# Kernel tuning notes

Hardware: AMD Instinct MI355X
Metric: run time of the kernel (lower is better)

The kernel has to match this reference:

```python
import jax, jax.numpy as jnp
import numpy as np
import math

B, L, H, V, NH, HD, FF, NL = 4096, 64, 64, 21, 4, 16, 128, 2


def _ln(x, g, b, eps=1e-6):
    mu = jnp.mean(x, axis=-1, keepdims=True)
    var = jnp.mean(jnp.square(x - mu), axis=-1, keepdims=True)
    return g * (x - mu) * jax.lax.rsqrt(var + eps) + b


def _pe():
    # standard sinusoidal positional encoding (L, H)
    pos = np.arange(L, dtype=np.float32)[:, None]
    div = np.exp(np.arange(0, H, 2, dtype=np.float32) * (-math.log(10000.0) / H))
    pe = np.zeros((L, H), dtype=np.float32)
    pe[:, 0::2] = np.sin(pos * div)
    pe[:, 1::2] = np.cos(pos * div)
    return jnp.asarray(pe)


def _soft_assemble(soft_mask, digit_values):
    # differentiable base-10 assembly: weight digit i by 10^(#digits to its right)
    cum = jnp.cumsum(soft_mask, axis=1)
    tot = jnp.sum(soft_mask, axis=1, keepdims=True)
    w = jnp.power(10.0, (tot - cum) * soft_mask) * soft_mask
    return jnp.sum(digit_values * w, axis=1, keepdims=True)  # (B,1)


def _fixed_ops(l, r):
    add = l + r
    sub = l - r
    mul = l * r
    bad = jnp.abs(r) < 1e-6
    div = jnp.where(bad, 0.0, l / jnp.where(bad, 1.0, r))
    ones = jnp.ones_like(l)
    dvalid = (~bad).astype(l.dtype)
    results = jnp.stack([add, sub, mul, div], axis=1)   # (B,4,1)
    valids = jnp.stack([ones, ones, ones, dvalid], axis=1)
    return results, valids


def _forward(token_ids, emb, np_w, np_b, grp_wq, grp_bq, grp_wk, grp_bk, grp_ln_g, grp_ln_b,
             attn_w, attn_b, ln1_g, ln1_b, ln2_g, ln2_b, ffn_w1, ffn_b1, ffn_w2, ffn_b2,
             enc_g, enc_b, red_w, red_b, opc_w, opc_b, res_w, res_b, soft_op):
    mask = (token_ids != 0).astype(jnp.float32)                     # (B,L)
    idsf = token_ids.astype(jnp.float32)
    is_digit = ((token_ids >= 4) & (token_ids <= 13)).astype(jnp.float32)
    digit_values = (idsf - 4.0) * is_digit
    is_op = (token_ids >= 14) & (token_ids <= 17)
    op_type = jnp.where(is_op, idsf - 13.0, 0.0)                    # 14->1 .. 17->4
    is_operator = is_op.astype(jnp.float32)
    num_feat = jnp.stack([digit_values, is_digit, op_type, is_operator], axis=-1)  # (B,L,4)

    x = emb[token_ids] * math.sqrt(H) + num_feat @ np_w + np_b      # (B,L,H)
    x = x + _pe()

    eye = jnp.eye(L, dtype=jnp.float32)
    adj = jnp.eye(L, k=1, dtype=jnp.float32) + jnp.eye(L, k=-1, dtype=jnp.float32)
    tri = jnp.triu(jnp.ones((L, L), jnp.float32))
    a_up = jnp.eye(L, k=1, dtype=jnp.float32)
    pairmask = mask[:, :, None] * mask[:, None, :]

    prior = jnp.float32(0.0)
    for i in range(NL):
        # --- Tree-Transformer group (constituent) attention ---
        c = _ln(x, grp_ln_g[i], grp_ln_b[i])
        q = c @ grp_wq[i] + grp_bq[i]
        k = c @ grp_wk[i] + grp_bk[i]
        s = jnp.einsum('bid,bjd->bij', q, k) / math.sqrt(H)
        gm = adj[None] * pairmask
        s = jnp.where(gm > 0, s, -1e9)
        nb = jax.nn.softmax(s, axis=-1)
        nb = jnp.sqrt(nb * jnp.swapaxes(nb, -1, -2) + 1e-9)
        nb = prior + (1.0 - prior) * nb
        t = (jnp.log(nb + 1e-9) * a_up[None]) @ tri
        g = jnp.exp(tri @ t) * (tri - eye)[None]
        g = g + jnp.swapaxes(g, -1, -2) + jnp.where(eye[None] > 0, nb, 1e-9)  # (B,L,L)
        # --- multi-head attention weighted by group prob (pre-norm residual) ---
        h = _ln(x, ln1_g[i], ln1_b[i])
        def proj(w, b):
            return (h @ w + b).reshape(B, L, NH, HD).transpose(0, 2, 1, 3)
        qh, kh, vh = proj(attn_w[i, 0], attn_b[i, 0]), proj(attn_w[i, 1], attn_b[i, 1]), proj(attn_w[i, 2], attn_b[i, 2])
        sc = jnp.einsum('bhid,bhjd->bhij', qh, kh) / math.sqrt(HD)
        sc = jnp.where(mask[:, None, None, :] > 0, sc, -1e9)
        p = jax.nn.softmax(sc, axis=-1) * g[:, None]
        o = jnp.einsum('bhij,bhjd->bhid', p, vh).transpose(0, 2, 1, 3).reshape(B, L, H)
        x = x + (o @ attn_w[i, 3] + attn_b[i, 3])
        # --- FFN ---
        h2 = _ln(x, ln2_g[i], ln2_b[i])
        x = x + (jax.nn.relu(h2 @ ffn_w1[i] + ffn_b1[i]) @ ffn_w2[i] + ffn_b2[i])
        prior = g

    x = _ln(x, enc_g, enc_b)
    scores = jnp.squeeze(x @ red_w + red_b, -1) + (1.0 - mask) * -1e9
    rw = jax.nn.softmax(scores, axis=-1)                            # reduction weights (B,L)
    cum = jnp.cumsum(rw, axis=1)
    left_mask = (1.0 - cum) * is_digit
    right_mask = (cum - rw) * is_digit
    left_val = _soft_assemble(left_mask, digit_values)
    right_val = _soft_assemble(right_mask, digit_values)
    pooled = jnp.sum(x * rw[..., None], axis=1)                     # (B,H)
    op_logits = pooled @ opc_w + opc_b
    op_probs = jax.nn.softmax(op_logits, axis=-1)
    all_res, all_val = _fixed_ops(left_val, right_val)
    if soft_op:
        w = op_probs[..., None]
    else:
        w = jax.nn.one_hot(jnp.argmax(op_probs, axis=-1), 4)[..., None]
    result = jnp.sum(all_res * w, axis=1)                           # (B,1)
    valid = jnp.sum(all_val * w, axis=1)
    rc = jnp.sign(result) * jnp.log1p(jnp.abs(result))
    result_embedding = jnp.concatenate([rc, valid], axis=-1) @ res_w + res_b  # (B,H)
    return result, result_embedding, valid, left_val, right_val, op_logits, rw


def setup_inputs() -> dict:
    key = jax.random.key(0)
    ks = jax.random.split(key, 16)
    s = 0.05
    rn = lambda k, shape: jax.random.normal(k, shape, dtype=jnp.float32) * s
    z = lambda shape: jnp.zeros(shape, jnp.float32)
    o = lambda shape: jnp.ones(shape, jnp.float32)
    return {
        'token_ids': jax.random.randint(ks[0], (B, L), 0, V, dtype=jnp.int32),
        'emb': rn(ks[1], (V, H)),
        'np_w': rn(ks[2], (4, H)), 'np_b': z((H,)),
        'grp_wq': rn(ks[3], (NL, H, H)), 'grp_bq': z((NL, H)),
        'grp_wk': rn(ks[4], (NL, H, H)), 'grp_bk': z((NL, H)),
        'grp_ln_g': o((NL, H)), 'grp_ln_b': z((NL, H)),
        'attn_w': rn(ks[5], (NL, 4, H, H)), 'attn_b': z((NL, 4, H)),
        'ln1_g': o((NL, H)), 'ln1_b': z((NL, H)),
        'ln2_g': o((NL, H)), 'ln2_b': z((NL, H)),
        'ffn_w1': rn(ks[6], (NL, H, FF)), 'ffn_b1': z((NL, FF)),
        'ffn_w2': rn(ks[7], (NL, FF, H)), 'ffn_b2': z((NL, H)),
        'enc_g': o((H,)), 'enc_b': z((H,)),
        'red_w': rn(ks[8], (H, 1)), 'red_b': z((1,)),
        'opc_w': rn(ks[9], (H, 4)), 'opc_b': z((4,)),
        'res_w': rn(ks[10], (2, H)), 'res_b': z((H,)),
    }


def reference(token_ids, emb, np_w, np_b, grp_wq, grp_bq, grp_wk, grp_bk, grp_ln_g, grp_ln_b,
              attn_w, attn_b, ln1_g, ln1_b, ln2_g, ln2_b, ffn_w1, ffn_b1, ffn_w2, ffn_b2,
              enc_g, enc_b, red_w, red_b, opc_w, opc_b, res_w, res_b):
    # inference path (training=None): hard argmax op select
    return _forward(token_ids, emb, np_w, np_b, grp_wq, grp_bq, grp_wk, grp_bk, grp_ln_g, grp_ln_b,
                    attn_w, attn_b, ln1_g, ln1_b, ln2_g, ln2_b, ffn_w1, ffn_b1, ffn_w2, ffn_b2,
                    enc_g, enc_b, red_w, red_b, opc_w, opc_b, res_w, res_b, soft_op=False)
```

## Files before the change

### kernel.cpp

```cpp
#include <hip/hip_runtime.h>
#include <math.h>

constexpr int BATCH = 4096;

constexpr int A    = 0;
constexpr int B0   = 4352;
constexpr int PS   = B0;
constexpr int PSQ  = B0 + 256;
constexpr int BH   = B0 + 512;
constexpr int MB   = 9024;
constexpr int M_MASK = MB + 0;
constexpr int M_DVAL = MB + 64;
constexpr int M_ISD  = MB + 128;
constexpr int M_SD   = MB + 192;
constexpr int M_NBU  = MB + 256;
constexpr int M_DG   = MB + 320;
constexpr int M_DVEC = MB + 384;
constexpr int M_S    = MB + 448;
constexpr int M_PRU  = MB + 512;
constexpr int M_PRD  = MB + 576;
constexpr int M_SU   = MB + 640;
constexpr int M_SDN  = MB + 704;
constexpr int LDSN   = MB + 768;

constexpr int O_RES   = 0;
constexpr int O_REMB  = 4096;
constexpr int O_VALID = 266240;
constexpr int O_LEFT  = 270336;
constexpr int O_RIGHT = 274432;
constexpr int O_OPL   = 278528;
constexpr int O_RW    = 294912;

#define LN_STORE(GPTR, BPTR, STORE) do {                                  \
    float s_ = 0.f, q_ = 0.f;                                             \
    _Pragma("unroll") for (int j = 0; j < 16; ++j) {                      \
        s_ += xr[j]; q_ = fmaf(xr[j], xr[j], q_); }                       \
    lds[PS  + (wv << 6) + lane] = s_;                                     \
    lds[PSQ + (wv << 6) + lane] = q_;                                     \
    __syncthreads();                                                      \
    float fs_ = lds[PS + lane] + lds[PS + 64 + lane]                      \
              + lds[PS + 128 + lane] + lds[PS + 192 + lane];              \
    float fq_ = lds[PSQ + lane] + lds[PSQ + 64 + lane]                    \
              + lds[PSQ + 128 + lane] + lds[PSQ + 192 + lane];            \
    float mu_ = fs_ * 0.015625f;                                          \
    float inv_ = rsqrtf(fq_ * 0.015625f - mu_ * mu_ + 1e-6f);             \
    _Pragma("unroll") for (int j = 0; j < 16; ++j) {                      \
        int c_ = c0 + j;                                                  \
        float hv_ = (xr[j] - mu_) * inv_ * (GPTR)[c_] + (BPTR)[c_];       \
        STORE;                                                            \
    }                                                                     \
    __syncthreads();                                                      \
} while (0)

__global__ void __launch_bounds__(256, 4) fsa_kernel(
    const int* __restrict__ tok,
    const float* __restrict__ emb, const float* __restrict__ np_w, const float* __restrict__ np_b,
    const float* __restrict__ grp_wq, const float* __restrict__ grp_bq,
    const float* __restrict__ grp_wk, const float* __restrict__ grp_bk,
    const float* __restrict__ grp_ln_g, const float* __restrict__ grp_ln_b,
    const float* __restrict__ attn_w, const float* __restrict__ attn_b,
    const float* __restrict__ ln1_g, const float* __restrict__ ln1_b,
    const float* __restrict__ ln2_g, const float* __restrict__ ln2_b,
    const float* __restrict__ ffn_w1, const float* __restrict__ ffn_b1,
    const float* __restrict__ ffn_w2, const float* __restrict__ ffn_b2,
    const float* __restrict__ enc_g, const float* __restrict__ enc_b,
    const float* __restrict__ red_w, const float* __restrict__ red_b,
    const float* __restrict__ opc_w, const float* __restrict__ opc_b,
    const float* __restrict__ res_w, const float* __restrict__ res_b,
    float* __restrict__ out)
{
    __shared__ __align__(16) float lds[LDSN];
    const int b = blockIdx.x;
    const int tid = threadIdx.x;
    const int lane = tid & 63;
    const int wv = __builtin_amdgcn_readfirstlane(tid >> 6);
    const int c0 = wv << 4;
    float xr[16];

    {
        int t = tok[(b << 6) + lane];
        float mk  = (t != 0) ? 1.f : 0.f;
        float isd = (t >= 4 && t <= 13) ? 1.f : 0.f;
        float dvv = ((float)t - 4.f) * isd;
        float iso = (t >= 14 && t <= 17) ? 1.f : 0.f;
        float opt = iso * ((float)t - 13.f);
        if (wv == 0) {
            lds[M_MASK + lane] = mk;  lds[M_DVAL + lane] = dvv; lds[M_ISD + lane] = isd;
            lds[M_PRU + lane] = 0.f;  lds[M_PRD + lane] = 0.f;
        }
        const float lg = -0.143911568f;
        #pragma unroll
        for (int j = 0; j < 16; ++j) {
            int c = c0 + j;
            float freq = expf((float)(c & ~1) * lg);
            float ang = (float)lane * freq;
            float pe = (c & 1) ? cosf(ang) : sinf(ang);
            xr[j] = emb[t * 64 + c] * 8.f
                  + dvv * np_w[c] + isd * np_w[64 + c]
                  + opt * np_w[128 + c] + iso * np_w[192 + c]
                  + np_b[c] + pe;
        }
    }
    __syncthreads();
    const unsigned long long mall = __ballot(lds[M_MASK + lane] > 0.f);

    for (int il = 0; il < 2; ++il) {
        const float* gwq = grp_wq + il * 4096; const float* gbq = grp_bq + (il << 6);
        const float* gwk = grp_wk + il * 4096; const float* gbk = grp_bk + (il << 6);
        const float* glg = grp_ln_g + (il << 6); const float* glb = grp_ln_b + (il << 6);
        const float* aw  = attn_w + il * 16384;  const float* ab  = attn_b + (il << 8);
        const float* l1g = ln1_g + (il << 6);    const float* l1b = ln1_b + (il << 6);
        const float* l2g = ln2_g + (il << 6);    const float* l2b = ln2_b + (il << 6);
        const float* fw1 = ffn_w1 + il * 8192;   const float* fb1 = ffn_b1 + (il << 7);
        const float* fw2 = ffn_w2 + il * 8192;   const float* fb2 = ffn_b2 + (il << 6);

        LN_STORE(glg, glb, lds[A + c_ * 64 + lane] = hv_);
        {
            float qa[16], ka[16];
            #pragma unroll
            for (int j = 0; j < 16; ++j) { qa[j] = gbq[c0 + j]; ka[j] = gbk[c0 + j]; }
            #pragma unroll 8
            for (int kk = 0; kk < 64; ++kk) {
                float a = lds[A + kk * 64 + lane];
                const float* wq = gwq + kk * 64 + c0;
                const float* wk = gwk + kk * 64 + c0;
                #pragma unroll
                for (int j = 0; j < 16; ++j) {
                    qa[j] = fmaf(a, wq[j], qa[j]);
                    ka[j] = fmaf(a, wk[j], ka[j]);
                }
            }
            #pragma unroll
            for (int j = 0; j < 16; ++j) lds[B0 + (c0 + j) * 64 + lane] = qa[j];
            __syncthreads();
            #pragma unroll
            for (int j = 0; j < 16; ++j) lds[A + (c0 + j) * 64 + lane] = ka[j];
            __syncthreads();
        }

        if (tid < 126) {
            int i = tid >> 1, w = tid & 1;
            int ra = w ? i + 1 : i, rb = w ? i : i + 1;
            float s = 0.f;
            #pragma unroll 8
            for (int c2 = 0; c2 < 64; ++c2)
                s = fmaf(lds[B0 + c2 * 64 + ra], lds[A + c2 * 64 + rb], s);
            lds[(w ? M_SDN : M_SU) + i] = s * 0.125f;
        }
        __syncthreads();

        if (wv == 0) {
            const int i = lane;
            float mi  = lds[M_MASK + i];
            float mup = (i < 63) ? lds[M_MASK + i + 1] : 0.f;
            float mdn = (i > 0)  ? lds[M_MASK + i - 1] : 0.f;
            float eu = (mi > 0.f && mup > 0.f) ? lds[M_SU + i] : -1e9f;
            float ed = (i > 0 && mi > 0.f && mdn > 0.f) ? lds[M_SDN + i - 1] : -1e9f;
            float m = fmaxf(eu, ed);
            float nu, nd, ng;
            if (m <= -1e9f) { nu = 0.015625f; nd = 0.015625f; ng = 0.015625f; }
            else {
                float zu = __expf(eu - m), zd = __expf(ed - m);
                float iz = 1.f / (zu + zd);
                nu = zu * iz; nd = zd * iz; ng = 0.f;
            }
            float nd1 = __shfl_down(nd, 1);
            float pd = lds[M_PRD + i];
            float dsym = sqrtf(ng * ng + 1e-9f);
            float d2 = pd + (1.f - pd) * dsym;
            lds[M_DVEC + i] = d2; lds[M_PRD + i] = d2;
            float la = 0.f;
            if (i < 63) {
                float pu = lds[M_PRU + i];
                float as_ = sqrtf(nu * nd1 + 1e-9f);
                float a2 = pu + (1.f - pu) * as_;
                la = logf(a2 + 1e-9f);
                lds[M_PRU + i] = __expf(la) + 1e-9f;
            }
            float x = __shfl_up(la, 1);
            if (i == 0) x = 0.f;
            #pragma unroll
            for (int off = 1; off < 64; off <<= 1) {
                float t2 = __shfl_up(x, off);
                if (i >= off) x += t2;
            }
            lds[M_S + i] = x;
        }
        __syncthreads();

        LN_STORE(l1g, l1b, lds[A + c_ * 64 + lane] = hv_);
        {
            const int hb = wv << 4;
            const int TB = B0 + wv * 640;
            const int jl = lane & 15, cq = lane >> 4;
            float qa[16];
            #pragma unroll
            for (int j = 0; j < 16; ++j) qa[j] = ab[hb + j];
            #pragma unroll 8
            for (int kk = 0; kk < 64; ++kk) {
                float a = lds[A + kk * 64 + lane];
                const float* wq = aw + kk * 64 + hb;
                #pragma unroll
                for (int j = 0; j < 16; ++j) qa[j] = fmaf(a, wq[j], qa[j]);
            }
            float o[16];
            #pragma unroll
            for (int c = 0; c < 16; ++c) o[c] = 0.f;
            float mrun = -1e30f, z = 0.f;
            for (int jt = 0; jt < 4; ++jt) {
                {
                    float kacc[4], vacc[4];
                    #pragma unroll
                    for (int j = 0; j < 4; ++j) {
                        kacc[j] = ab[64 + hb + (cq << 2) + j];
                        vacc[j] = ab[128 + hb + (cq << 2) + j];
                    }
                    const int row = (jt << 4) + jl;
                    #pragma unroll 8
                    for (int kk = 0; kk < 64; ++kk) {
                        float a = lds[A + kk * 64 + row];
                        const float* wk  = aw + 4096 + kk * 64 + hb + (cq << 2);
                        const float* wvp = aw + 8192 + kk * 64 + hb + (cq << 2);
                        #pragma unroll
                        for (int j = 0; j < 4; ++j) {
                            kacc[j] = fmaf(a, wk[j], kacc[j]);
                            vacc[j] = fmaf(a, wvp[j], vacc[j]);
                        }
                    }
                    *reinterpret_cast<float4*>(&lds[TB + jl * 20 + (cq << 2)]) =
                        make_float4(kacc[0], kacc[1], kacc[2], kacc[3]);
                    *reinterpret_cast<float4*>(&lds[TB + 320 + jl * 20 + (cq << 2)]) =
                        make_float4(vacc[0], vacc[1], vacc[2], vacc[3]);
                    asm volatile("s_waitcnt lgkmcnt(0)" ::: "memory");
                }
                #pragma unroll
                for (int half = 0; half < 2; ++half) {
                    float sc[8]; float tm = -1e30f;
                    #pragma unroll
                    for (int jj = 0; jj < 8; ++jj) {
                        const int jloc = (half << 3) + jj;
                        const int j = (jt << 4) + jloc;
                        float s = 0.f;
                        #pragma unroll
                        for (int c4 = 0; c4 < 4; ++c4) {
                            const float4 kv = *reinterpret_cast<const float4*>(
                                &lds[TB + jloc * 20 + (c4 << 2)]);
                            s = fmaf(qa[(c4<<2)+0], kv.x, s); s = fmaf(qa[(c4<<2)+1], kv.y, s);
                            s = fmaf(qa[(c4<<2)+2], kv.z, s); s = fmaf(qa[(c4<<2)+3], kv.w, s);
                        }
                        s = ((mall >> j) & 1ull) ? s * 0.25f : -1e9f;
                        sc[jj] = s; tm = fmaxf(tm, s);
                    }
                    float mn = fmaxf(mrun, tm);
                    float rs = __expf(mrun - mn);
                    z *= rs;
                    #pragma unroll
                    for (int c = 0; c < 16; ++c) o[c] *= rs;
                    mrun = mn;
                    float Sr  = lds[M_S + lane];
                    float dvr = lds[M_DVEC + lane];
                    #pragma unroll
                    for (int jj = 0; jj < 8; ++jj) {
                        const int jloc = (half << 3) + jj;
                        const int j = (jt << 4) + jloc;
                        float e = __expf(sc[jj] - mn);
                        z += e;
                        float Sj = lds[M_S + j];
                        float g = (j == lane) ? dvr
                                  : (__expf((j > lane) ? (Sj - Sr) : (Sr - Sj)) + 1e-9f);
                        float w = e * g;
                        #pragma unroll
                        for (int c4 = 0; c4 < 4; ++c4) {
                            const float4 vv = *reinterpret_cast<const float4*>(
                                &lds[TB + 320 + jloc * 20 + (c4 << 2)]);
                            o[(c4<<2)+0] = fmaf(w, vv.x, o[(c4<<2)+0]);
                            o[(c4<<2)+1] = fmaf(w, vv.y, o[(c4<<2)+1]);
                            o[(c4<<2)+2] = fmaf(w, vv.z, o[(c4<<2)+2]);
                            o[(c4<<2)+3] = fmaf(w, vv.w, o[(c4<<2)+3]);
                        }
                    }
                }
            }
            float iz = 1.f / z;
            __syncthreads();
            #pragma unroll
            for (int c = 0; c < 16; ++c) lds[A + lane * 65 + hb + c] = o[c] * iz;
            __syncthreads();
            const float* Wo = aw + 12288; const float* bo = ab + 192;
            float acc[16];
            #pragma unroll
            for (int j = 0; j < 16; ++j) acc[j] = bo[c0 + j];
            #pragma unroll 8
            for (int dd = 0; dd < 64; ++dd) {
                float a = lds[A + lane * 65 + dd];
                const float* wr = Wo + dd * 64 + c0;
                #pragma unroll
                for (int j = 0; j < 16; ++j) acc[j] = fmaf(a, wr[j], acc[j]);
            }
            #pragma unroll
            for (int j = 0; j < 16; ++j) xr[j] += acc[j];
        }
        __syncthreads();

        LN_STORE(l2g, l2b, lds[A + c_ * 64 + lane] = hv_);
        {
            float fa[16];
            #pragma unroll
            for (int j = 0; j < 16; ++j) fa[j] = fb1[c0 + j];
            #pragma unroll 8
            for (int kk = 0; kk < 64; ++kk) {
                float a = lds[A + kk * 64 + lane];
                const float* wr = fw1 + kk * 128 + c0;
                #pragma unroll
                for (int j = 0; j < 16; ++j) fa[j] = fmaf(a, wr[j], fa[j]);
            }
            #pragma unroll
            for (int j = 0; j < 16; ++j) lds[B0 + (c0 + j) * 64 + lane] = fmaxf(fa[j], 0.f);
        }
        __syncthreads();
        {
            float acc[16];
            #pragma unroll
            for (int j = 0; j < 16; ++j) acc[j] = fb2[c0 + j];
            #pragma unroll 8
            for (int kk = 0; kk < 64; ++kk) {
                float a = lds[B0 + kk * 64 + lane];
                const float* wr = fw2 + kk * 64 + c0;
                #pragma unroll
                for (int j = 0; j < 16; ++j) acc[j] = fmaf(a, wr[j], acc[j]);
            }
            #pragma unroll
            for (int j = 0; j < 16; ++j) xr[j] += acc[j];
        }
        __syncthreads();
        {
            float fa[16];
            #pragma unroll
            for (int j = 0; j < 16; ++j) fa[j] = fb1[64 + c0 + j];
            #pragma unroll 8
            for (int kk = 0; kk < 64; ++kk) {
                float a = lds[A + kk * 64 + lane];
                const float* wr = fw1 + kk * 128 + 64 + c0;
                #pragma unroll
                for (int j = 0; j < 16; ++j) fa[j] = fmaf(a, wr[j], fa[j]);
            }
            #pragma unroll
            for (int j = 0; j < 16; ++j) lds[B0 + (c0 + j) * 64 + lane] = fmaxf(fa[j], 0.f);
        }
        __syncthreads();
        {
            float acc[16];
            #pragma unroll
            for (int j = 0; j < 16; ++j) acc[j] = 0.f;
            #pragma unroll 8
            for (int kk = 0; kk < 64; ++kk) {
                float a = lds[B0 + kk * 64 + lane];
                const float* wr = fw2 + (64 + kk) * 64 + c0;
                #pragma unroll
                for (int j = 0; j < 16; ++j) acc[j] = fmaf(a, wr[j], acc[j]);
            }
            #pragma unroll
            for (int j = 0; j < 16; ++j) xr[j] += acc[j];
        }
        __syncthreads();
    }

    LN_STORE(enc_g, enc_b, lds[BH + lane * 65 + c_] = hv_);
    if (tid < 64) {
        float s = 0.f;
        #pragma unroll 8
        for (int c2 = 0; c2 < 64; ++c2)
            s = fmaf(lds[BH + tid * 65 + c2], red_w[c2], s);
        s += red_b[0];
        s += (1.f - lds[M_MASK + tid]) * -1e9f;
        lds[M_SU + tid] = s;
    }
    __syncthreads();

    if (wv == 0) {
        float s = lds[M_SU + lane];
        float m = s;
        #pragma unroll
        for (int off = 1; off < 64; off <<= 1) m = fmaxf(m, __shfl_xor(m, off));
        float ee = expf(s - m);
        float z = ee;
        #pragma unroll
        for (int off = 1; off < 64; off <<= 1) z += __shfl_xor(z, off);
        float rw = ee / z;
        lds[M_SD + lane] = rw;
        float cum = rw;
        #pragma unroll
        for (int off = 1; off < 64; off <<= 1) { float t2 = __shfl_up(cum, off); if (lane >= off) cum += t2; }
        float isd = lds[M_ISD + lane], dvv = lds[M_DVAL + lane];
        float lm = (1.f - cum) * isd;
        float rm = (cum - rw) * isd;
        float cl = lm;
        #pragma unroll
        for (int off = 1; off < 64; off <<= 1) { float t2 = __shfl_up(cl, off); if (lane >= off) cl += t2; }
        float totl = __shfl(cl, 63);
        float wL = powf(10.f, (totl - cl) * lm) * lm;
        float lv = dvv * wL;
        #pragma unroll
        for (int off = 1; off < 64; off <<= 1) lv += __shfl_xor(lv, off);
        float cr = rm;
        #pragma unroll
        for (int off = 1; off < 64; off <<= 1) { float t2 = __shfl_up(cr, off); if (lane >= off) cr += t2; }
        float totr = __shfl(cr, 63);
        float wR = powf(10.f, (totr - cr) * rm) * rm;
        float rv = dvv * wR;
        #pragma unroll
        for (int off = 1; off < 64; off <<= 1) rv += __shfl_xor(rv, off);
        if (lane == 0) { lds[M_DG + 2] = lv; lds[M_DG + 3] = rv; }
    }
    __syncthreads();

    if (tid < 64) {
        float p = 0.f;
        #pragma unroll 8
        for (int r2 = 0; r2 < 64; ++r2)
            p = fmaf(lds[BH + r2 * 65 + tid], lds[M_SD + r2], p);
        lds[M_NBU + tid] = p;
    }
    __syncthreads();
    if (tid < 4) {
        float s = opc_b[tid];
        for (int c2 = 0; c2 < 64; ++c2) s = fmaf(lds[M_NBU + c2], opc_w[(c2 << 2) + tid], s);
        lds[M_DG + 4 + tid] = s;
    }
    __syncthreads();
    if (tid == 0) {
        float l = lds[M_DG + 2], r = lds[M_DG + 3];
        float o0 = lds[M_DG + 4], o1 = lds[M_DG + 5], o2 = lds[M_DG + 6], o3 = lds[M_DG + 7];
        int op = 0; float bm = o0;
        if (o1 > bm) { bm = o1; op = 1; }
        if (o2 > bm) { bm = o2; op = 2; }
        if (o3 > bm) { bm = o3; op = 3; }
        float res, vl = 1.f;
        if (op == 0)      res = l + r;
        else if (op == 1) res = l - r;
        else if (op == 2) res = l * r;
        else { bool bad = fabsf(r) < 1e-6f; res = bad ? 0.f : (l / r); vl = bad ? 0.f : 1.f; }
        float rc = (res > 0.f) ? log1pf(res) : ((res < 0.f) ? -log1pf(-res) : 0.f);
        lds[M_DG + 0] = rc; lds[M_DG + 1] = vl;
        out[O_RES + b]   = res;
        out[O_VALID + b] = vl;
        out[O_LEFT + b]  = l;
        out[O_RIGHT + b] = r;
    }
    __syncthreads();
    if (tid < 64) {
        float rc = lds[M_DG + 0], vl = lds[M_DG + 1];
        out[O_REMB + (b << 6) + tid] = rc * res_w[tid] + vl * res_w[64 + tid] + res_b[tid];
        out[O_RW + (b << 6) + tid] = lds[M_SD + tid];
    }
    if (tid >= 64 && tid < 68) {
        int o = tid - 64;
        out[O_OPL + (b << 2) + o] = lds[M_DG + 4 + o];
    }
}

extern "C" void kernel_launch(void* const* d_in, const int* in_sizes, int n_in,
                              void* d_out, int out_size, void* d_ws, size_t ws_size,
                              hipStream_t stream)
{
    fsa_kernel<<<dim3(BATCH), dim3(256), 0, stream>>>(
        (const int*)d_in[0],
        (const float*)d_in[1],  (const float*)d_in[2],  (const float*)d_in[3],
        (const float*)d_in[4],  (const float*)d_in[5],  (const float*)d_in[6],  (const float*)d_in[7],
        (const float*)d_in[8],  (const float*)d_in[9],  (const float*)d_in[10], (const float*)d_in[11],
        (const float*)d_in[12], (const float*)d_in[13], (const float*)d_in[14], (const float*)d_in[15],
        (const float*)d_in[16], (const float*)d_in[17], (const float*)d_in[18], (const float*)d_in[19],
        (const float*)d_in[20], (const float*)d_in[21], (const float*)d_in[22], (const float*)d_in[23],
        (const float*)d_in[24], (const float*)d_in[25], (const float*)d_in[26], (const float*)d_in[27],
        (float*)d_out);
}
```

Before: 950.4 us.

## Fuse layernorm partial sums into producers, use exp2 softmax, fold op-classifier into readout

Each layernorm's partial-sum pass now runs at the end of the stage that produced x, which removes one block-wide barrier per layernorm. The attention softmax and group-gate exponentials switch to exp2f with the scale folded into a log2e constant. The final pooling and op-classifier matmuls are reassociated: the per-row opc projections are computed together with the reduction scores and then weighted by the readout vector inside a single wave, which removes two barrier-separated serial stages. This adds extra register pressure and relies on the M_S values being stored in log2 units for exp2 to stay equivalent.

```diff
diff --git a/kernel.cpp b/kernel.cpp
--- a/kernel.cpp
+++ b/kernel.cpp
@@ -5,15 +5,14 @@
 
 constexpr int A    = 0;
 constexpr int B0   = 4352;
-constexpr int PS   = B0;
-constexpr int PSQ  = B0 + 256;
-constexpr int BH   = B0 + 512;
+constexpr int PS   = B0 + 4096;
+constexpr int PSQ  = PS + 256;
+constexpr int HOPB = PS;
 constexpr int MB   = 9024;
 constexpr int M_MASK = MB + 0;
 constexpr int M_DVAL = MB + 64;
 constexpr int M_ISD  = MB + 128;
 constexpr int M_SD   = MB + 192;
-constexpr int M_NBU  = MB + 256;
 constexpr int M_DG   = MB + 320;
 constexpr int M_DVEC = MB + 384;
 constexpr int M_S    = MB + 448;
@@ -31,13 +30,15 @@
 constexpr int O_OPL   = 278528;
 constexpr int O_RW    = 294912;
 
-#define LN_STORE(GPTR, BPTR, STORE) do {                                  \
+#define LN_PART() do {                                                    \
     float s_ = 0.f, q_ = 0.f;                                             \
     _Pragma("unroll") for (int j = 0; j < 16; ++j) {                      \
         s_ += xr[j]; q_ = fmaf(xr[j], xr[j], q_); }                       \
     lds[PS  + (wv << 6) + lane] = s_;                                     \
     lds[PSQ + (wv << 6) + lane] = q_;                                     \
-    __syncthreads();                                                      \
+} while (0)
+
+#define LN_APPLY(GPTR, BPTR) do {                                         \
     float fs_ = lds[PS + lane] + lds[PS + 64 + lane]                      \
               + lds[PS + 128 + lane] + lds[PS + 192 + lane];              \
     float fq_ = lds[PSQ + lane] + lds[PSQ + 64 + lane]                    \
@@ -46,10 +47,9 @@
     float inv_ = rsqrtf(fq_ * 0.015625f - mu_ * mu_ + 1e-6f);             \
     _Pragma("unroll") for (int j = 0; j < 16; ++j) {                      \
         int c_ = c0 + j;                                                  \
-        float hv_ = (xr[j] - mu_) * inv_ * (GPTR)[c_] + (BPTR)[c_];       \
-        STORE;                                                            \
+        lds[A + c_ * 64 + lane] =                                         \
+            (xr[j] - mu_) * inv_ * (GPTR)[c_] + (BPTR)[c_];               \
     }                                                                     \
-    __syncthreads();                                                      \
 } while (0)
 
 __global__ void __launch_bounds__(256, 4) fsa_kernel(
@@ -100,6 +100,7 @@
                   + opt * np_w[128 + c] + iso * np_w[192 + c]
                   + np_b[c] + pe;
         }
+        LN_PART();
     }
     __syncthreads();
     const unsigned long long mall = __ballot(lds[M_MASK + lane] > 0.f);
@@ -114,9 +115,11 @@
         const float* fw1 = ffn_w1 + il * 8192;   const float* fb1 = ffn_b1 + (il << 7);
         const float* fw2 = ffn_w2 + il * 8192;   const float* fb2 = ffn_b2 + (il << 6);
 
-        LN_STORE(glg, glb, lds[A + c_ * 64 + lane] = hv_);
-        {
-            float qa[16], ka[16];
+        LN_APPLY(glg, glb);
+        __syncthreads();
+        float ka[16];
+        {
+            float qa[16];
             #pragma unroll
             for (int j = 0; j < 16; ++j) { qa[j] = gbq[c0 + j]; ka[j] = gbk[c0 + j]; }
             #pragma unroll 8
@@ -132,11 +135,11 @@
             }
             #pragma unroll
             for (int j = 0; j < 16; ++j) lds[B0 + (c0 + j) * 64 + lane] = qa[j];
-            __syncthreads();
-            #pragma unroll
-            for (int j = 0; j < 16; ++j) lds[A + (c0 + j) * 64 + lane] = ka[j];
-            __syncthreads();
-        }
+        }
+        __syncthreads();
+        #pragma unroll
+        for (int j = 0; j < 16; ++j) lds[A + (c0 + j) * 64 + lane] = ka[j];
+        __syncthreads();
 
         if (tid < 126) {
             int i = tid >> 1, w = tid & 1;
@@ -149,6 +152,7 @@
         }
         __syncthreads();
 
+        LN_PART();
         if (wv == 0) {
             const int i = lane;
             float mi  = lds[M_MASK + i];
@@ -169,15 +173,15 @@
             float dsym = sqrtf(ng * ng + 1e-9f);
             float d2 = pd + (1.f - pd) * dsym;
             lds[M_DVEC + i] = d2; lds[M_PRD + i] = d2;
-            float la = 0.f;
+            float la2 = 0.f;
             if (i < 63) {
                 float pu = lds[M_PRU + i];
                 float as_ = sqrtf(nu * nd1 + 1e-9f);
                 float a2 = pu + (1.f - pu) * as_;
-                la = logf(a2 + 1e-9f);
-                lds[M_PRU + i] = __expf(la) + 1e-9f;
-            }
-            float x = __shfl_up(la, 1);
+                la2 = __log2f(a2 + 1e-9f);
+                lds[M_PRU + i] = exp2f(la2) + 1e-9f;
+            }
+            float x = __shfl_up(la2, 1);
             if (i == 0) x = 0.f;
             #pragma unroll
             for (int off = 1; off < 64; off <<= 1) {
@@ -188,11 +192,13 @@
         }
         __syncthreads();
 
-        LN_STORE(l1g, l1b, lds[A + c_ * 64 + lane] = hv_);
+        LN_APPLY(l1g, l1b);
+        __syncthreads();
         {
             const int hb = wv << 4;
             const int TB = B0 + wv * 640;
             const int jl = lane & 15, cq = lane >> 4;
+            const float SCL = 0.36067376f;
             float qa[16];
             #pragma unroll
             for (int j = 0; j < 16; ++j) qa[j] = ab[hb + j];
@@ -203,6 +209,8 @@
                 #pragma unroll
                 for (int j = 0; j < 16; ++j) qa[j] = fmaf(a, wq[j], qa[j]);
             }
+            const float Sr2 = lds[M_S + lane];
+            const float dvr = lds[M_DVEC + lane];
             float o[16];
             #pragma unroll
             for (int c = 0; c < 16; ++c) o[c] = 0.f;
@@ -248,26 +256,24 @@
                             s = fmaf(qa[(c4<<2)+0], kv.x, s); s = fmaf(qa[(c4<<2)+1], kv.y, s);
                             s = fmaf(qa[(c4<<2)+2], kv.z, s); s = fmaf(qa[(c4<<2)+3], kv.w, s);
                         }
-                        s = ((mall >> j) & 1ull) ? s * 0.25f : -1e9f;
+                        s = ((mall >> j) & 1ull) ? s * SCL : -1e9f;
                         sc[jj] = s; tm = fmaxf(tm, s);
                     }
                     float mn = fmaxf(mrun, tm);
-                    float rs = __expf(mrun - mn);
+                    float rs = exp2f(mrun - mn);
                     z *= rs;
                     #pragma unroll
                     for (int c = 0; c < 16; ++c) o[c] *= rs;
                     mrun = mn;
-                    float Sr  = lds[M_S + lane];
-                    float dvr = lds[M_DVEC + lane];
                     #pragma unroll
                     for (int jj = 0; jj < 8; ++jj) {
                         const int jloc = (half << 3) + jj;
                         const int j = (jt << 4) + jloc;
-                        float e = __expf(sc[jj] - mn);
+                        float e = exp2f(sc[jj] - mn);
                         z += e;
-                        float Sj = lds[M_S + j];
+                        float Sj2 = lds[M_S + j];
                         float g = (j == lane) ? dvr
-                                  : (__expf((j > lane) ? (Sj - Sr) : (Sr - Sj)) + 1e-9f);
+                                  : (exp2f((j > lane) ? (Sj2 - Sr2) : (Sr2 - Sj2)) + 1e-9f);
                         float w = e * g;
                         #pragma unroll
                         for (int c4 = 0; c4 < 4; ++c4) {
@@ -299,10 +305,12 @@
             }
             #pragma unroll
             for (int j = 0; j < 16; ++j) xr[j] += acc[j];
-        }
-        __syncthreads();
-
-        LN_STORE(l2g, l2b, lds[A + c_ * 64 + lane] = hv_);
+            LN_PART();
+        }
+        __syncthreads();
+
+        LN_APPLY(l2g, l2b);
+        __syncthreads();
         {
             float fa[16];
             #pragma unroll
@@ -361,19 +369,28 @@
             }
             #pragma unroll
             for (int j = 0; j < 16; ++j) xr[j] += acc[j];
+            LN_PART();
         }
         __syncthreads();
     }
 
-    LN_STORE(enc_g, enc_b, lds[BH + lane * 65 + c_] = hv_);
+    LN_APPLY(enc_g, enc_b);
+    __syncthreads();
     if (tid < 64) {
-        float s = 0.f;
+        float s = 0.f, h0 = 0.f, h1 = 0.f, h2 = 0.f, h3 = 0.f;
         #pragma unroll 8
-        for (int c2 = 0; c2 < 64; ++c2)
-            s = fmaf(lds[BH + tid * 65 + c2], red_w[c2], s);
+        for (int c2 = 0; c2 < 64; ++c2) {
+            float hv = lds[A + c2 * 64 + tid];
+            s  = fmaf(hv, red_w[c2], s);
+            h0 = fmaf(hv, opc_w[(c2 << 2) + 0], h0);
+            h1 = fmaf(hv, opc_w[(c2 << 2) + 1], h1);
+            h2 = fmaf(hv, opc_w[(c2 << 2) + 2], h2);
+            h3 = fmaf(hv, opc_w[(c2 << 2) + 3], h3);
+        }
         s += red_b[0];
         s += (1.f - lds[M_MASK + tid]) * -1e9f;
         lds[M_SU + tid] = s;
+        *reinterpret_cast<float4*>(&lds[HOPB + (tid << 2)]) = make_float4(h0, h1, h2, h3);
     }
     __syncthreads();
 
@@ -410,52 +427,42 @@
         float rv = dvv * wR;
         #pragma unroll
         for (int off = 1; off < 64; off <<= 1) rv += __shfl_xor(rv, off);
-        if (lane == 0) { lds[M_DG + 2] = lv; lds[M_DG + 3] = rv; }
-    }
-    __syncthreads();
-
-    if (tid < 64) {
-        float p = 0.f;
-        #pragma unroll 8
-        for (int r2 = 0; r2 < 64; ++r2)
-            p = fmaf(lds[BH + r2 * 65 + tid], lds[M_SD + r2], p);
-        lds[M_NBU + tid] = p;
-    }
-    __syncthreads();
-    if (tid < 4) {
-        float s = opc_b[tid];
-        for (int c2 = 0; c2 < 64; ++c2) s = fmaf(lds[M_NBU + c2], opc_w[(c2 << 2) + tid], s);
-        lds[M_DG + 4 + tid] = s;
-    }
-    __syncthreads();
-    if (tid == 0) {
-        float l = lds[M_DG + 2], r = lds[M_DG + 3];
-        float o0 = lds[M_DG + 4], o1 = lds[M_DG + 5], o2 = lds[M_DG + 6], o3 = lds[M_DG + 7];
-        int op = 0; float bm = o0;
-        if (o1 > bm) { bm = o1; op = 1; }
-        if (o2 > bm) { bm = o2; op = 2; }
-        if (o3 > bm) { bm = o3; op = 3; }
-        float res, vl = 1.f;
-        if (op == 0)      res = l + r;
-        else if (op == 1) res = l - r;
-        else if (op == 2) res = l * r;
-        else { bool bad = fabsf(r) < 1e-6f; res = bad ? 0.f : (l / r); vl = bad ? 0.f : 1.f; }
-        float rc = (res > 0.f) ? log1pf(res) : ((res < 0.f) ? -log1pf(-res) : 0.f);
-        lds[M_DG + 0] = rc; lds[M_DG + 1] = vl;
-        out[O_RES + b]   = res;
-        out[O_VALID + b] = vl;
-        out[O_LEFT + b]  = l;
-        out[O_RIGHT + b] = r;
+        float4 hop = *reinterpret_cast<const float4*>(&lds[HOPB + (lane << 2)]);
+        float p0 = rw * hop.x, p1 = rw * hop.y, p2 = rw * hop.z, p3 = rw * hop.w;
+        #pragma unroll
+        for (int off = 1; off < 64; off <<= 1) {
+            p0 += __shfl_xor(p0, off); p1 += __shfl_xor(p1, off);
+            p2 += __shfl_xor(p2, off); p3 += __shfl_xor(p3, off);
+        }
+        if (lane == 0) {
+            float o0 = p0 + opc_b[0], o1 = p1 + opc_b[1];
+            float o2 = p2 + opc_b[2], o3 = p3 + opc_b[3];
+            int op = 0; float bm = o0;
+            if (o1 > bm) { bm = o1; op = 1; }
+            if (o2 > bm) { bm = o2; op = 2; }
+            if (o3 > bm) { bm = o3; op = 3; }
+            float l = lv, r = rv, res, vl = 1.f;
+            if (op == 0)      res = l + r;
+            else if (op == 1) res = l - r;
+            else if (op == 2) res = l * r;
+            else { bool bad = fabsf(r) < 1e-6f; res = bad ? 0.f : (l / r); vl = bad ? 0.f : 1.f; }
+            float rc = (res > 0.f) ? log1pf(res) : ((res < 0.f) ? -log1pf(-res) : 0.f);
+            lds[M_DG + 0] = rc; lds[M_DG + 1] = vl;
+            out[O_RES + b]   = res;
+            out[O_VALID + b] = vl;
+            out[O_LEFT + b]  = l;
+            out[O_RIGHT + b] = r;
+            out[O_OPL + (b << 2) + 0] = o0;
+            out[O_OPL + (b << 2) + 1] = o1;
+            out[O_OPL + (b << 2) + 2] = o2;
+            out[O_OPL + (b << 2) + 3] = o3;
+        }
     }
     __syncthreads();
     if (tid < 64) {
         float rc = lds[M_DG + 0], vl = lds[M_DG + 1];
         out[O_REMB + (b << 6) + tid] = rc * res_w[tid] + vl * res_w[64 + tid] + res_b[tid];
         out[O_RW + (b << 6) + tid] = lds[M_SD + tid];
-    }
-    if (tid >= 64 && tid < 68) {
-        int o = tid - 64;
-        out[O_OPL + (b << 2) + o] = lds[M_DG + 4 + o];
     }
 }
 
```

After: 957.6 us. No clear change (+0.8%).
